# Performance work log

Measured on AMD Instinct MI355X. Metric: run time of the kernel, lower is better.

The kernel has to match this reference:

```python
import jax, jax.numpy as jnp
import numpy as np

N = 100000      # n_nodes
E = 1600000     # n_edges (avg degree 16)
D_IN, D_H, D_OUT = 128, 64, 16


def setup_inputs() -> dict:
    key = jax.random.key(0)
    k1, k2, k3, k4 = jax.random.split(key, 4)
    x = jax.random.normal(k1, (N, D_IN), dtype=jnp.float32)
    edge_index = jax.random.randint(k2, (2, E), 0, N, dtype=jnp.int32)
    W1 = jax.random.normal(k3, (D_IN, D_H), dtype=jnp.float32) / np.sqrt(D_IN)
    b1 = jnp.zeros((D_H,), dtype=jnp.float32)
    W2 = jax.random.normal(k4, (D_H, D_OUT), dtype=jnp.float32) / np.sqrt(D_H)
    b2 = jnp.zeros((D_OUT,), dtype=jnp.float32)
    return {"x": x, "edge_index": edge_index, "W1": W1, "b1": b1, "W2": W2, "b2": b2}


def gcn_conv(x, src, dst, W, b, n):
    """PyG GCNConv: linear transform, then deg^-1/2 A deg^-1/2 aggregation, + bias.
    src/dst already include self-loops."""
    h = x @ W                                              # [n, d_out]
    deg = jax.ops.segment_sum(jnp.ones_like(dst, dtype=h.dtype), dst, num_segments=n)
    dinv = jnp.where(deg > 0, jax.lax.rsqrt(jnp.maximum(deg, 1.0)), 0.0)
    norm = dinv[src] * dinv[dst]                           # [E+n]
    msgs = h[src] * norm[:, None]                          # gather + scale
    out = jax.ops.segment_sum(msgs, dst, num_segments=n)   # scatter-add
    return out + b


def reference(x, edge_index, W1, b1, W2, b2):
    loops = jnp.arange(N, dtype=edge_index.dtype)
    src = jnp.concatenate([edge_index[0], loops])
    dst = jnp.concatenate([edge_index[1], loops])
    h = jax.nn.relu(gcn_conv(x, src, dst, W1, b1, N))
    return gcn_conv(h, src, dst, W2, b2, N)
```

## Files before the change

### kernel.cpp

```cpp
#include <hip/hip_runtime.h>
#include <cstdint>

#define N_NODES 100000
#define N_EDGES 1600000
#define D_IN    128
#define D_H     64
#define D_OUT   16
#define M_TILES 6250

#define NBKT   512
#define NPB    196
#define BCAP   4096
#define TILE_E 4096
#define NTILES ((N_EDGES + TILE_E - 1) / TILE_E)
#define G1     128

typedef __attribute__((ext_vector_type(8))) short short8;
typedef __attribute__((ext_vector_type(4))) float floatx4;

static __device__ __forceinline__ unsigned short f2bf(float f) {
    unsigned int u = __float_as_uint(f);
    u = u + 0x7FFFu + ((u >> 16) & 1u);
    return (unsigned short)(u >> 16);
}
static __device__ __forceinline__ float bf2f(unsigned short h) {
    return __uint_as_float(((unsigned int)h) << 16);
}


__global__ __launch_bounds__(512) void zero_small_kernel(int* __restrict__ cursors,
                                                         int* __restrict__ srcs) {
    cursors[threadIdx.x] = 0;
    if (threadIdx.x < 16) srcs[N_EDGES + threadIdx.x] = 0;
}

__global__ __launch_bounds__(256) void bin_kernel(const int* __restrict__ src,
                                                  const int* __restrict__ dst,
                                                  int* __restrict__ cursors,
                                                  int* __restrict__ region) {
    __shared__ int hcnt[NBKT];
    __shared__ int hbase[NBKT];
    const int t = threadIdx.x;
    for (int tile = blockIdx.x; tile < NTILES; tile += gridDim.x) {
        for (int i = t; i < NBKT; i += 256) hcnt[i] = 0;
        __syncthreads();
        int e0 = tile * TILE_E + t * 16;
        int pk[16], bk[16], rk[16];
        bool full = (e0 + 16 <= N_EDGES);
        if (full) {
            const int4* dp = (const int4*)(dst + e0);
            const int4* sp = (const int4*)(src + e0);
            int dv[16], sv[16];
            #pragma unroll
            for (int q = 0; q < 4; ++q) {
                int4 d4 = dp[q]; int4 s4 = sp[q];
                dv[4*q+0]=d4.x; dv[4*q+1]=d4.y; dv[4*q+2]=d4.z; dv[4*q+3]=d4.w;
                sv[4*q+0]=s4.x; sv[4*q+1]=s4.y; sv[4*q+2]=s4.z; sv[4*q+3]=s4.w;
            }
            #pragma unroll
            for (int k = 0; k < 16; ++k) {
                int d = dv[k];
                int b = d / NPB;
                bk[k] = b;
                pk[k] = ((d - b * NPB) << 17) | sv[k];
                rk[k] = atomicAdd(&hcnt[b], 1);
            }
        }
        __syncthreads();
        for (int i = t; i < NBKT; i += 256) {
            int c = hcnt[i];
            if (c > 0) hbase[i] = atomicAdd(&cursors[i], c);
        }
        __syncthreads();
        if (full) {
            #pragma unroll
            for (int k = 0; k < 16; ++k)
                region[bk[k] * BCAP + hbase[bk[k]] + rk[k]] = pk[k];
        }
        __syncthreads();
    }
}

__global__ __launch_bounds__(256) void build_kernel(const int* __restrict__ cursors,
                                                    const int* __restrict__ region,
                                                    int* __restrict__ offsets,
                                                    float* __restrict__ dinv,
                                                    int* __restrict__ srcs) {
    __shared__ int lhist[NPB];
    __shared__ int lscan[NPB + 1];
    __shared__ int sbuf[256];
    __shared__ int srt[BCAP];
    __shared__ int red[4];
    int b = blockIdx.x;
    int t = threadIdx.x;

    int c0 = cursors[t];
    int c1 = cursors[t + 256];
    int p = ((t < b) ? c0 : 0) + ((t + 256 < b) ? c1 : 0);
    int lane = t & 63, wid = t >> 6;
    #pragma unroll
    for (int off = 32; off > 0; off >>= 1) p += __shfl_down(p, off);
    if (lane == 0) red[wid] = p;
    __syncthreads();
    int base = red[0] + red[1] + red[2] + red[3];
    int cnt = cursors[b];
    const int* reg = region + b * BCAP;

    for (int i = t; i < NPB; i += 256) lhist[i] = 0;
    __syncthreads();
    for (int i = t; i < cnt; i += 256) {
        int ln = reg[i] >> 17;
        atomicAdd(&lhist[ln], 1);
    }
    __syncthreads();
    int v = (t < NPB) ? lhist[t] : 0;
    sbuf[t] = v;
    __syncthreads();
    for (int off = 1; off < 256; off <<= 1) {
        int u = (t >= off) ? sbuf[t - off] : 0;
        __syncthreads();
        sbuf[t] += u;
        __syncthreads();
    }
    int incl = sbuf[t];
    if (t < NPB) lscan[t] = incl - v;
    if (t == NPB - 1) lscan[NPB] = incl;
    __syncthreads();
    if (t < NPB) lhist[t] = incl - v;
    __syncthreads();

    int node0 = b * NPB;
    int nlim = N_NODES - node0;
    if (nlim > NPB) nlim = NPB;
    if (t < nlim) {
        offsets[node0 + t] = base + lscan[t];
        int c = lscan[t + 1] - lscan[t];
        dinv[node0 + t] = rsqrtf((float)c + 1.0f);
    }
    if (b == (N_NODES - 1) / NPB && t == 0) offsets[N_NODES] = base + cnt;

    for (int i = t; i < cnt; i += 256) {
        int pk = reg[i];
        int ln = pk >> 17;
        int pos = atomicAdd(&lhist[ln], 1);
        srt[pos] = pk & 0x1FFFF;
    }
    __syncthreads();
    for (int i = t; i < cnt; i += 256) srcs[base + i] = srt[i];
}

__global__ __launch_bounds__(256) void gemm1_mfma_kernel(const float* __restrict__ x,
                                                         const float* __restrict__ W1,
                                                         const float* __restrict__ dinv,
                                                         unsigned short* __restrict__ hs) {
    __shared__ unsigned short bhi_lds[8192];
    __shared__ unsigned short blo_lds[8192];

    for (int e = threadIdx.x; e < 8192; e += 256) {
        int j    = e & 7;
        int lane = (e >> 3) & 63;
        int pair = e >> 9;
        int kc   = pair >> 2;
        int nt   = pair & 3;
        int k = kc * 32 + (lane >> 4) * 8 + j;
        int n = nt * 16 + (lane & 15);
        float w = W1[k * D_H + n];
        unsigned short hi = f2bf(w);
        float lo = w - bf2f(hi);
        bhi_lds[e] = hi;
        blo_lds[e] = f2bf(lo);
    }
    __syncthreads();

    int wid  = threadIdx.x >> 6;
    int lane = threadIdx.x & 63;
    int quad = lane >> 4;
    int m    = lane & 15;

    int tile = blockIdx.x * 4 + wid;
    if (tile >= M_TILES) return;
    int mbase = tile * 16;

    const float* xr = x + (size_t)(mbase + m) * D_IN + quad * 8;
    short8 ahi[4], alo[4];
    #pragma unroll
    for (int kc = 0; kc < 4; ++kc) {
        floatx4 v0 = *(const floatx4*)(xr + kc * 32);
        floatx4 v1 = *(const floatx4*)(xr + kc * 32 + 4);
        float f[8] = {v0.x, v0.y, v0.z, v0.w, v1.x, v1.y, v1.z, v1.w};
        #pragma unroll
        for (int j = 0; j < 8; ++j) {
            unsigned short hi = f2bf(f[j]);
            float lo = f[j] - bf2f(hi);
            ahi[kc][j] = (short)hi;
            alo[kc][j] = (short)f2bf(lo);
        }
    }

    floatx4 acc[4] = {{0.f,0.f,0.f,0.f},{0.f,0.f,0.f,0.f},{0.f,0.f,0.f,0.f},{0.f,0.f,0.f,0.f}};
    #pragma unroll
    for (int kc = 0; kc < 4; ++kc) {
        #pragma unroll
        for (int nt = 0; nt < 4; ++nt) {
            int fo = ((kc * 4 + nt) * 64 + lane) * 8;
            short8 bhi = *(const short8*)&bhi_lds[fo];
            short8 blo = *(const short8*)&blo_lds[fo];
            acc[nt] = __builtin_amdgcn_mfma_f32_16x16x32_bf16(ahi[kc], bhi, acc[nt], 0, 0, 0);
            acc[nt] = __builtin_amdgcn_mfma_f32_16x16x32_bf16(ahi[kc], blo, acc[nt], 0, 0, 0);
            acc[nt] = __builtin_amdgcn_mfma_f32_16x16x32_bf16(alo[kc], bhi, acc[nt], 0, 0, 0);
        }
    }

    float dv[4];
    #pragma unroll
    for (int r = 0; r < 4; ++r) dv[r] = dinv[mbase + quad * 4 + r];
    #pragma unroll
    for (int nt = 0; nt < 4; ++nt) {
        int col = nt * 16 + m;
        #pragma unroll
        for (int r = 0; r < 4; ++r) {
            int row = mbase + quad * 4 + r;
            hs[row * D_H + col] = f2bf(acc[nt][r] * dv[r]);
        }
    }
}

__global__ __launch_bounds__(256) void agg1_fused_kernel(const unsigned short* __restrict__ hs,
                                                         const int* __restrict__ offsets,
                                                         const int* __restrict__ srcs,
                                                         const float* __restrict__ dinv,
                                                         const float* __restrict__ b1,
                                                         const float* __restrict__ W2,
                                                         float* __restrict__ h2s) {
    __shared__ float rbuf[256];
    int wid  = threadIdx.x >> 6;
    int lane = threadIdx.x & 63;
    int wave = (blockIdx.x * blockDim.x + threadIdx.x) >> 6;
    int nwaves = (gridDim.x * blockDim.x) >> 6;

    int q = lane >> 4;
    int c = lane & 15;
    float w2c[16];
    #pragma unroll
    for (int j = 0; j < 16; ++j) w2c[j] = W2[(q * 16 + j) * D_OUT + c];
    float bias = b1[lane];
    float* myr = &rbuf[wid * 64];

    for (int node = wave; node < N_NODES; node += nwaves) {
        int beg = __builtin_amdgcn_readfirstlane(offsets[node]);
        int end = __builtin_amdgcn_readfirstlane(offsets[node + 1]);
        float acc = bf2f(hs[node * D_H + lane]);
        for (int e = beg; e < end; e += 16) {
            int rem = end - e;
            const int* ep = srcs + e;
            int jj[16];
            #pragma unroll
            for (int k = 0; k < 16; ++k)
                jj[k] = __builtin_amdgcn_readfirstlane(ep[k]);
            float vv[16];
            #pragma unroll
            for (int k = 0; k < 16; ++k) {
                const unsigned short* hp = hs + (size_t)jj[k] * D_H;
                vv[k] = bf2f(hp[lane]);
            }
            #pragma unroll
            for (int k = 0; k < 16; ++k) {
                float m = (k < rem) ? 1.0f : 0.0f;
                acc = fmaf(vv[k], m, acc);
            }
        }
        float dv = dinv[node];
        float r = fmaxf(acc * dv + bias, 0.f);

        myr[lane] = r;
        float part = 0.f;
        #pragma unroll
        for (int j = 0; j < 16; ++j) part += myr[q * 16 + j] * w2c[j];
        part += __shfl_xor(part, 16);
        part += __shfl_xor(part, 32);
        if (lane < 16) h2s[node * D_OUT + lane] = part * dv;
    }
}

__global__ __launch_bounds__(256) void agg2_kernel(const float* __restrict__ h2s,
                                                   const int* __restrict__ offsets,
                                                   const int* __restrict__ srcs,
                                                   const float* __restrict__ dinv,
                                                   const float* __restrict__ b2,
                                                   float* __restrict__ out) {
    int col = threadIdx.x & 15;
    int nidx = (blockIdx.x * blockDim.x + threadIdx.x) >> 4;
    int stride = (gridDim.x * blockDim.x) >> 4;
    for (int node = nidx; node < N_NODES; node += stride) {
        int beg = offsets[node], end = offsets[node + 1];
        float acc = h2s[node * D_OUT + col];
        for (int e = beg; e < end; e += 16) {
            int rem = end - e;
            const int* ep = srcs + e;
            int jj[16];
            #pragma unroll
            for (int k = 0; k < 16; ++k) jj[k] = ep[k];
            float vv[16];
            #pragma unroll
            for (int k = 0; k < 16; ++k) vv[k] = h2s[jj[k] * D_OUT + col];
            #pragma unroll
            for (int k = 0; k < 16; ++k) {
                float m = (k < rem) ? 1.0f : 0.0f;
                acc = fmaf(vv[k], m, acc);
            }
        }
        out[node * D_OUT + col] = acc * dinv[node] + b2[col];
    }
}

extern "C" void kernel_launch(void* const* d_in, const int* in_sizes, int n_in,
                              void* d_out, int out_size, void* d_ws, size_t ws_size,
                              hipStream_t stream) {
    const float* x  = (const float*)d_in[0];
    const int*   ei = (const int*)d_in[1];
    const float* W1 = (const float*)d_in[2];
    const float* b1 = (const float*)d_in[3];
    const float* W2 = (const float*)d_in[4];
    const float* b2 = (const float*)d_in[5];
    float* out = (float*)d_out;

    const int* src = ei;
    const int* dst = ei + N_EDGES;

    char* w = (char*)d_ws;
    int*   cursors  = (int*)(w + 0);
    int*   offsets  = (int*)(w + 4096);
    float* dinv     = (float*)(w + 404224);
    int*   srcs     = (int*)(w + 804224);
    unsigned short* hs = (unsigned short*)(w + 7204352);
    float* h2s      = (float*)(w + 20004480);
    int*   region   = (int*)(w + 26404480);

    zero_small_kernel<<<1, 512, 0, stream>>>(cursors, srcs);
    bin_kernel<<<G1, 256, 0, stream>>>(src, dst, cursors, region);
    build_kernel<<<NBKT, 256, 0, stream>>>(cursors, region, offsets, dinv, srcs);
    gemm1_mfma_kernel<<<(M_TILES + 3) / 4, 256, 0, stream>>>(x, W1, dinv, hs);
    agg1_fused_kernel<<<6250, 256, 0, stream>>>(hs, offsets, srcs, dinv, b1, W2, h2s);
    agg2_kernel<<<6250, 256, 0, stream>>>(h2s, offsets, srcs, dinv, b2, out);
}
```

Measured before the change: 206.4 us.

## Fuse all GCN stages into one cooperative persistent kernel with grid syncs

Replaces the six-kernel pipeline with a single cooperative mega-kernel that runs zeroing, edge binning, CSR build, the first GEMM and both aggregations, separated by grid.sync. Bucket count doubles, nodes per bucket halve and edges per thread drop, so binning runs one tile per block across 1024 blocks. W1 is split into bf16 hi/lo parts once into global memory rather than in LDS per block. The aim is to remove launch gaps and inter-kernel drain, at the cost of grid-wide barriers, persistent-loop load imbalance and reading W1 fragments from global/L2. A fallback multi-kernel path runs if a cooperative launch is not possible.

```diff
diff --git a/kernel.cpp b/kernel.cpp
--- a/kernel.cpp
+++ b/kernel.cpp
@@ -1,5 +1,8 @@
 #include <hip/hip_runtime.h>
+#include <hip/hip_cooperative_groups.h>
 #include <cstdint>
+
+namespace cg = cooperative_groups;
 
 #define N_NODES 100000
 #define N_EDGES 1600000
@@ -8,12 +11,13 @@
 #define D_OUT   16
 #define M_TILES 6250
 
-#define NBKT   512
-#define NPB    196
-#define BCAP   4096
-#define TILE_E 4096
-#define NTILES ((N_EDGES + TILE_E - 1) / TILE_E)
-#define G1     128
+#define NBKT   1024
+#define NPB    98
+#define BCAP   2048
+#define EPT    8
+#define TILE_E 2048
+#define NTILES 782
+#define GRID_B 1024
 
 typedef __attribute__((ext_vector_type(8))) short short8;
 typedef __attribute__((ext_vector_type(4))) float floatx4;
@@ -28,64 +32,331 @@
 }
 
 
-__global__ __launch_bounds__(512) void zero_small_kernel(int* __restrict__ cursors,
-                                                         int* __restrict__ srcs) {
+union SMem {
+    struct { int hcnt[NBKT]; int hbase[NBKT]; } bin;
+    struct { int lhist[NPB]; int lscan[NPB + 1]; int sbuf[256]; int red[4];
+             int srt[BCAP]; } bld;
+    float rbuf[256];
+};
+
+__global__ __launch_bounds__(256, 4) void mega_kernel(
+        const float* __restrict__ x,
+        const int* __restrict__ esrc, const int* __restrict__ edst,
+        const float* __restrict__ W1, const float* __restrict__ b1,
+        const float* __restrict__ W2, const float* __restrict__ b2,
+        float* __restrict__ out,
+        int* __restrict__ cursors, int* __restrict__ offsets,
+        float* __restrict__ dinv, int* __restrict__ srcs,
+        unsigned short* __restrict__ hs, float* __restrict__ h2s,
+        int* __restrict__ region,
+        unsigned short* __restrict__ w1hi, unsigned short* __restrict__ w1lo) {
+    cg::grid_group grid = cg::this_grid();
+    __shared__ SMem sm;
+    const int t = threadIdx.x;
+    const int gtid = blockIdx.x * 256 + t;
+
+    if (gtid < NBKT) cursors[gtid] = 0;
+    if (gtid < 16) srcs[N_EDGES + gtid] = 0;
+    if (gtid < 8192) {
+        int e = gtid;
+        int j    = e & 7;
+        int lane = (e >> 3) & 63;
+        int pair = e >> 9;
+        int kc   = pair >> 2;
+        int nt   = pair & 3;
+        int k = kc * 32 + (lane >> 4) * 8 + j;
+        int n = nt * 16 + (lane & 15);
+        float w = W1[k * D_H + n];
+        unsigned short hi = f2bf(w);
+        w1hi[e] = hi;
+        w1lo[e] = f2bf(w - bf2f(hi));
+    }
+    grid.sync();
+
+    {
+        int tile = blockIdx.x;
+        if (tile < NTILES) {
+            for (int i = t; i < NBKT; i += 256) sm.bin.hcnt[i] = 0;
+            __syncthreads();
+            int e0 = tile * TILE_E + t * EPT;
+            int pk[EPT], bk[EPT], rk[EPT];
+            bool full = (e0 + EPT <= N_EDGES);
+            if (full) {
+                const int4* dp = (const int4*)(edst + e0);
+                const int4* sp = (const int4*)(esrc + e0);
+                int dv[EPT], sv[EPT];
+                #pragma unroll
+                for (int q = 0; q < EPT / 4; ++q) {
+                    int4 d4 = dp[q]; int4 s4 = sp[q];
+                    dv[4*q+0]=d4.x; dv[4*q+1]=d4.y; dv[4*q+2]=d4.z; dv[4*q+3]=d4.w;
+                    sv[4*q+0]=s4.x; sv[4*q+1]=s4.y; sv[4*q+2]=s4.z; sv[4*q+3]=s4.w;
+                }
+                #pragma unroll
+                for (int k = 0; k < EPT; ++k) {
+                    int d = dv[k];
+                    int b = d / NPB;
+                    bk[k] = b;
+                    pk[k] = ((d - b * NPB) << 17) | sv[k];
+                    rk[k] = atomicAdd(&sm.bin.hcnt[b], 1);
+                }
+            }
+            __syncthreads();
+            for (int i = t; i < NBKT; i += 256) {
+                int c = sm.bin.hcnt[i];
+                if (c > 0) sm.bin.hbase[i] = atomicAdd(&cursors[i], c);
+            }
+            __syncthreads();
+            if (full) {
+                #pragma unroll
+                for (int k = 0; k < EPT; ++k)
+                    region[bk[k] * BCAP + sm.bin.hbase[bk[k]] + rk[k]] = pk[k];
+            }
+        }
+    }
+    grid.sync();
+
+    {
+        int b = blockIdx.x;
+        int p = 0;
+        #pragma unroll
+        for (int j = 0; j < 4; ++j) {
+            int i = t + 256 * j;
+            int cv = cursors[i];
+            p += (i < b) ? cv : 0;
+        }
+        int lane = t & 63, wid = t >> 6;
+        #pragma unroll
+        for (int off = 32; off > 0; off >>= 1) p += __shfl_down(p, off);
+        if (lane == 0) sm.bld.red[wid] = p;
+        __syncthreads();
+        int base = sm.bld.red[0] + sm.bld.red[1] + sm.bld.red[2] + sm.bld.red[3];
+        int cnt = cursors[b];
+        const int* reg = region + b * BCAP;
+
+        for (int i = t; i < NPB; i += 256) sm.bld.lhist[i] = 0;
+        __syncthreads();
+        for (int i = t; i < cnt; i += 256)
+            atomicAdd(&sm.bld.lhist[reg[i] >> 17], 1);
+        __syncthreads();
+        int v = (t < NPB) ? sm.bld.lhist[t] : 0;
+        sm.bld.sbuf[t] = v;
+        __syncthreads();
+        for (int off = 1; off < 256; off <<= 1) {
+            int u = (t >= off) ? sm.bld.sbuf[t - off] : 0;
+            __syncthreads();
+            sm.bld.sbuf[t] += u;
+            __syncthreads();
+        }
+        int incl = sm.bld.sbuf[t];
+        if (t < NPB) sm.bld.lscan[t] = incl - v;
+        if (t == NPB - 1) sm.bld.lscan[NPB] = incl;
+        __syncthreads();
+        if (t < NPB) sm.bld.lhist[t] = incl - v;
+        __syncthreads();
+
+        int node0 = b * NPB;
+        int nlim = N_NODES - node0;
+        if (nlim > NPB) nlim = NPB;
+        if (t < nlim) {
+            offsets[node0 + t] = base + sm.bld.lscan[t];
+            int c = sm.bld.lscan[t + 1] - sm.bld.lscan[t];
+            dinv[node0 + t] = rsqrtf((float)c + 1.0f);
+        }
+        if (b == (N_NODES - 1) / NPB && t == 0) offsets[N_NODES] = base + cnt;
+
+        for (int i = t; i < cnt; i += 256) {
+            int pk2 = reg[i];
+            int pos = atomicAdd(&sm.bld.lhist[pk2 >> 17], 1);
+            sm.bld.srt[pos] = pk2 & 0x1FFFF;
+        }
+        __syncthreads();
+        for (int i = t; i < cnt; i += 256) srcs[base + i] = sm.bld.srt[i];
+    }
+    grid.sync();
+
+    {
+        int wid  = t >> 6;
+        int lane = t & 63;
+        int quad = lane >> 4;
+        int m    = lane & 15;
+
+        for (int tile = blockIdx.x * 4 + wid; tile < M_TILES; tile += gridDim.x * 4) {
+            int mbase = tile * 16;
+            const float* xr = x + (size_t)(mbase + m) * D_IN + quad * 8;
+            short8 ahi[4], alo[4];
+            #pragma unroll
+            for (int kc = 0; kc < 4; ++kc) {
+                floatx4 v0 = *(const floatx4*)(xr + kc * 32);
+                floatx4 v1 = *(const floatx4*)(xr + kc * 32 + 4);
+                float f[8] = {v0.x, v0.y, v0.z, v0.w, v1.x, v1.y, v1.z, v1.w};
+                #pragma unroll
+                for (int j = 0; j < 8; ++j) {
+                    unsigned short hi = f2bf(f[j]);
+                    ahi[kc][j] = (short)hi;
+                    alo[kc][j] = (short)f2bf(f[j] - bf2f(hi));
+                }
+            }
+            floatx4 acc[4] = {{0.f,0.f,0.f,0.f},{0.f,0.f,0.f,0.f},{0.f,0.f,0.f,0.f},{0.f,0.f,0.f,0.f}};
+            #pragma unroll
+            for (int kc = 0; kc < 4; ++kc) {
+                #pragma unroll
+                for (int nt = 0; nt < 4; ++nt) {
+                    int fo = ((kc * 4 + nt) * 64 + lane) * 8;
+                    short8 bhi = *(const short8*)&w1hi[fo];
+                    short8 blo = *(const short8*)&w1lo[fo];
+                    acc[nt] = __builtin_amdgcn_mfma_f32_16x16x32_bf16(ahi[kc], bhi, acc[nt], 0, 0, 0);
+                    acc[nt] = __builtin_amdgcn_mfma_f32_16x16x32_bf16(ahi[kc], blo, acc[nt], 0, 0, 0);
+                    acc[nt] = __builtin_amdgcn_mfma_f32_16x16x32_bf16(alo[kc], bhi, acc[nt], 0, 0, 0);
+                }
+            }
+            float dv[4];
+            #pragma unroll
+            for (int r = 0; r < 4; ++r) dv[r] = dinv[mbase + quad * 4 + r];
+            #pragma unroll
+            for (int nt = 0; nt < 4; ++nt) {
+                int col = nt * 16 + m;
+                #pragma unroll
+                for (int r = 0; r < 4; ++r)
+                    hs[(mbase + quad * 4 + r) * D_H + col] = f2bf(acc[nt][r] * dv[r]);
+            }
+        }
+    }
+    grid.sync();
+
+    {
+        int wid  = t >> 6;
+        int lane = t & 63;
+        int wave = (blockIdx.x * 256 + t) >> 6;
+        const int nwaves = gridDim.x * 4;
+        int q = lane >> 4;
+        int c = lane & 15;
+        float w2c[16];
+        #pragma unroll
+        for (int j = 0; j < 16; ++j) w2c[j] = W2[(q * 16 + j) * D_OUT + c];
+        float bias = b1[lane];
+        float* myr = &sm.rbuf[wid * 64];
+
+        for (int node = wave; node < N_NODES; node += nwaves) {
+            int beg = __builtin_amdgcn_readfirstlane(offsets[node]);
+            int end = __builtin_amdgcn_readfirstlane(offsets[node + 1]);
+            float acc = bf2f(hs[node * D_H + lane]);
+            for (int e = beg; e < end; e += 16) {
+                int rem = end - e;
+                const int* ep = srcs + e;
+                int jj[16];
+                #pragma unroll
+                for (int k = 0; k < 16; ++k)
+                    jj[k] = __builtin_amdgcn_readfirstlane(ep[k]);
+                float vv[16];
+                #pragma unroll
+                for (int k = 0; k < 16; ++k) {
+                    const unsigned short* hp = hs + (size_t)jj[k] * D_H;
+                    vv[k] = bf2f(hp[lane]);
+                }
+                #pragma unroll
+                for (int k = 0; k < 16; ++k) {
+                    float m = (k < rem) ? 1.0f : 0.0f;
+                    acc = fmaf(vv[k], m, acc);
+                }
+            }
+            float dv = dinv[node];
+            float r = fmaxf(acc * dv + bias, 0.f);
+            myr[lane] = r;
+            float part = 0.f;
+            #pragma unroll
+            for (int j = 0; j < 16; ++j) part += myr[q * 16 + j] * w2c[j];
+            part += __shfl_xor(part, 16);
+            part += __shfl_xor(part, 32);
+            if (lane < 16) h2s[node * D_OUT + lane] = part * dv;
+        }
+    }
+    grid.sync();
+
+    {
+        int col = t & 15;
+        int nidx = (blockIdx.x * 256 + t) >> 4;
+        const int stride = (gridDim.x * 256) >> 4;
+        for (int node = nidx; node < N_NODES; node += stride) {
+            int beg = offsets[node], end = offsets[node + 1];
+            float acc = h2s[node * D_OUT + col];
+            for (int e = beg; e < end; e += 16) {
+                int rem = end - e;
+                const int* ep = srcs + e;
+                int jj[16];
+                #pragma unroll
+                for (int k = 0; k < 16; ++k) jj[k] = ep[k];
+                float vv[16];
+                #pragma unroll
+                for (int k = 0; k < 16; ++k) vv[k] = h2s[jj[k] * D_OUT + col];
+                #pragma unroll
+                for (int k = 0; k < 16; ++k) {
+                    float m = (k < rem) ? 1.0f : 0.0f;
+                    acc = fmaf(vv[k], m, acc);
+                }
+            }
+            out[node * D_OUT + col] = acc * dinv[node] + b2[col];
+        }
+    }
+}
+
+
+__global__ __launch_bounds__(1024) void fb_zero(int* __restrict__ cursors,
+                                                int* __restrict__ srcs) {
     cursors[threadIdx.x] = 0;
     if (threadIdx.x < 16) srcs[N_EDGES + threadIdx.x] = 0;
 }
 
-__global__ __launch_bounds__(256) void bin_kernel(const int* __restrict__ src,
-                                                  const int* __restrict__ dst,
-                                                  int* __restrict__ cursors,
-                                                  int* __restrict__ region) {
+__global__ __launch_bounds__(256) void fb_bin(const int* __restrict__ esrc,
+                                              const int* __restrict__ edst,
+                                              int* __restrict__ cursors,
+                                              int* __restrict__ region) {
     __shared__ int hcnt[NBKT];
     __shared__ int hbase[NBKT];
     const int t = threadIdx.x;
-    for (int tile = blockIdx.x; tile < NTILES; tile += gridDim.x) {
-        for (int i = t; i < NBKT; i += 256) hcnt[i] = 0;
-        __syncthreads();
-        int e0 = tile * TILE_E + t * 16;
-        int pk[16], bk[16], rk[16];
-        bool full = (e0 + 16 <= N_EDGES);
-        if (full) {
-            const int4* dp = (const int4*)(dst + e0);
-            const int4* sp = (const int4*)(src + e0);
-            int dv[16], sv[16];
-            #pragma unroll
-            for (int q = 0; q < 4; ++q) {
-                int4 d4 = dp[q]; int4 s4 = sp[q];
-                dv[4*q+0]=d4.x; dv[4*q+1]=d4.y; dv[4*q+2]=d4.z; dv[4*q+3]=d4.w;
-                sv[4*q+0]=s4.x; sv[4*q+1]=s4.y; sv[4*q+2]=s4.z; sv[4*q+3]=s4.w;
-            }
-            #pragma unroll
-            for (int k = 0; k < 16; ++k) {
-                int d = dv[k];
-                int b = d / NPB;
-                bk[k] = b;
-                pk[k] = ((d - b * NPB) << 17) | sv[k];
-                rk[k] = atomicAdd(&hcnt[b], 1);
-            }
-        }
-        __syncthreads();
-        for (int i = t; i < NBKT; i += 256) {
-            int c = hcnt[i];
-            if (c > 0) hbase[i] = atomicAdd(&cursors[i], c);
-        }
-        __syncthreads();
-        if (full) {
-            #pragma unroll
-            for (int k = 0; k < 16; ++k)
-                region[bk[k] * BCAP + hbase[bk[k]] + rk[k]] = pk[k];
-        }
-        __syncthreads();
-    }
-}
-
-__global__ __launch_bounds__(256) void build_kernel(const int* __restrict__ cursors,
-                                                    const int* __restrict__ region,
-                                                    int* __restrict__ offsets,
-                                                    float* __restrict__ dinv,
-                                                    int* __restrict__ srcs) {
+    int tile = blockIdx.x;
+    if (tile >= NTILES) return;
+    for (int i = t; i < NBKT; i += 256) hcnt[i] = 0;
+    __syncthreads();
+    int e0 = tile * TILE_E + t * EPT;
+    int pk[EPT], bk[EPT], rk[EPT];
+    bool full = (e0 + EPT <= N_EDGES);
+    if (full) {
+        const int4* dp = (const int4*)(edst + e0);
+        const int4* sp = (const int4*)(esrc + e0);
+        int dv[EPT], sv[EPT];
+        #pragma unroll
+        for (int q = 0; q < EPT / 4; ++q) {
+            int4 d4 = dp[q]; int4 s4 = sp[q];
+            dv[4*q+0]=d4.x; dv[4*q+1]=d4.y; dv[4*q+2]=d4.z; dv[4*q+3]=d4.w;
+            sv[4*q+0]=s4.x; sv[4*q+1]=s4.y; sv[4*q+2]=s4.z; sv[4*q+3]=s4.w;
+        }
+        #pragma unroll
+        for (int k = 0; k < EPT; ++k) {
+            int d = dv[k];
+            int b = d / NPB;
+            bk[k] = b;
+            pk[k] = ((d - b * NPB) << 17) | sv[k];
+            rk[k] = atomicAdd(&hcnt[b], 1);
+        }
+    }
+    __syncthreads();
+    for (int i = t; i < NBKT; i += 256) {
+        int c = hcnt[i];
+        if (c > 0) hbase[i] = atomicAdd(&cursors[i], c);
+    }
+    __syncthreads();
+    if (full) {
+        #pragma unroll
+        for (int k = 0; k < EPT; ++k)
+            region[bk[k] * BCAP + hbase[bk[k]] + rk[k]] = pk[k];
+    }
+}
+
+__global__ __launch_bounds__(256) void fb_build(const int* __restrict__ cursors,
+                                                const int* __restrict__ region,
+                                                int* __restrict__ offsets,
+                                                float* __restrict__ dinv,
+                                                int* __restrict__ srcs) {
     __shared__ int lhist[NPB];
     __shared__ int lscan[NPB + 1];
     __shared__ int sbuf[256];
@@ -93,10 +364,13 @@
     __shared__ int red[4];
     int b = blockIdx.x;
     int t = threadIdx.x;
-
-    int c0 = cursors[t];
-    int c1 = cursors[t + 256];
-    int p = ((t < b) ? c0 : 0) + ((t + 256 < b) ? c1 : 0);
+    int p = 0;
+    #pragma unroll
+    for (int j = 0; j < 4; ++j) {
+        int i = t + 256 * j;
+        int cv = cursors[i];
+        p += (i < b) ? cv : 0;
+    }
     int lane = t & 63, wid = t >> 6;
     #pragma unroll
     for (int off = 32; off > 0; off >>= 1) p += __shfl_down(p, off);
@@ -108,10 +382,7 @@
 
     for (int i = t; i < NPB; i += 256) lhist[i] = 0;
     __syncthreads();
-    for (int i = t; i < cnt; i += 256) {
-        int ln = reg[i] >> 17;
-        atomicAdd(&lhist[ln], 1);
-    }
+    for (int i = t; i < cnt; i += 256) atomicAdd(&lhist[reg[i] >> 17], 1);
     __syncthreads();
     int v = (t < NPB) ? lhist[t] : 0;
     sbuf[t] = v;
@@ -140,22 +411,20 @@
     if (b == (N_NODES - 1) / NPB && t == 0) offsets[N_NODES] = base + cnt;
 
     for (int i = t; i < cnt; i += 256) {
-        int pk = reg[i];
-        int ln = pk >> 17;
-        int pos = atomicAdd(&lhist[ln], 1);
-        srt[pos] = pk & 0x1FFFF;
+        int pk2 = reg[i];
+        int pos = atomicAdd(&lhist[pk2 >> 17], 1);
+        srt[pos] = pk2 & 0x1FFFF;
     }
     __syncthreads();
     for (int i = t; i < cnt; i += 256) srcs[base + i] = srt[i];
 }
 
-__global__ __launch_bounds__(256) void gemm1_mfma_kernel(const float* __restrict__ x,
-                                                         const float* __restrict__ W1,
-                                                         const float* __restrict__ dinv,
-                                                         unsigned short* __restrict__ hs) {
+__global__ __launch_bounds__(256) void fb_gemm1(const float* __restrict__ x,
+                                                const float* __restrict__ W1,
+                                                const float* __restrict__ dinv,
+                                                unsigned short* __restrict__ hs) {
     __shared__ unsigned short bhi_lds[8192];
     __shared__ unsigned short blo_lds[8192];
-
     for (int e = threadIdx.x; e < 8192; e += 256) {
         int j    = e & 7;
         int lane = (e >> 3) & 63;
@@ -166,21 +435,17 @@
         int n = nt * 16 + (lane & 15);
         float w = W1[k * D_H + n];
         unsigned short hi = f2bf(w);
-        float lo = w - bf2f(hi);
         bhi_lds[e] = hi;
-        blo_lds[e] = f2bf(lo);
-    }
-    __syncthreads();
-
+        blo_lds[e] = f2bf(w - bf2f(hi));
+    }
+    __syncthreads();
     int wid  = threadIdx.x >> 6;
     int lane = threadIdx.x & 63;
     int quad = lane >> 4;
     int m    = lane & 15;
-
     int tile = blockIdx.x * 4 + wid;
     if (tile >= M_TILES) return;
     int mbase = tile * 16;
-
     const float* xr = x + (size_t)(mbase + m) * D_IN + quad * 8;
     short8 ahi[4], alo[4];
     #pragma unroll
@@ -191,12 +456,10 @@
         #pragma unroll
         for (int j = 0; j < 8; ++j) {
             unsigned short hi = f2bf(f[j]);
-            float lo = f[j] - bf2f(hi);
             ahi[kc][j] = (short)hi;
-            alo[kc][j] = (short)f2bf(lo);
-        }
-    }
-
+            alo[kc][j] = (short)f2bf(f[j] - bf2f(hi));
+        }
+    }
     floatx4 acc[4] = {{0.f,0.f,0.f,0.f},{0.f,0.f,0.f,0.f},{0.f,0.f,0.f,0.f},{0.f,0.f,0.f,0.f}};
     #pragma unroll
     for (int kc = 0; kc < 4; ++kc) {
@@ -210,7 +473,6 @@
             acc[nt] = __builtin_amdgcn_mfma_f32_16x16x32_bf16(alo[kc], bhi, acc[nt], 0, 0, 0);
         }
     }
-
     float dv[4];
     #pragma unroll
     for (int r = 0; r < 4; ++r) dv[r] = dinv[mbase + quad * 4 + r];
@@ -218,26 +480,23 @@
     for (int nt = 0; nt < 4; ++nt) {
         int col = nt * 16 + m;
         #pragma unroll
-        for (int r = 0; r < 4; ++r) {
-            int row = mbase + quad * 4 + r;
-            hs[row * D_H + col] = f2bf(acc[nt][r] * dv[r]);
-        }
-    }
-}
-
-__global__ __launch_bounds__(256) void agg1_fused_kernel(const unsigned short* __restrict__ hs,
-                                                         const int* __restrict__ offsets,
-                                                         const int* __restrict__ srcs,
-                                                         const float* __restrict__ dinv,
-                                                         const float* __restrict__ b1,
-                                                         const float* __restrict__ W2,
-                                                         float* __restrict__ h2s) {
+        for (int r = 0; r < 4; ++r)
+            hs[(mbase + quad * 4 + r) * D_H + col] = f2bf(acc[nt][r] * dv[r]);
+    }
+}
+
+__global__ __launch_bounds__(256) void fb_agg1(const unsigned short* __restrict__ hs,
+                                               const int* __restrict__ offsets,
+                                               const int* __restrict__ srcs,
+                                               const float* __restrict__ dinv,
+                                               const float* __restrict__ b1,
+                                               const float* __restrict__ W2,
+                                               float* __restrict__ h2s) {
     __shared__ float rbuf[256];
     int wid  = threadIdx.x >> 6;
     int lane = threadIdx.x & 63;
     int wave = (blockIdx.x * blockDim.x + threadIdx.x) >> 6;
     int nwaves = (gridDim.x * blockDim.x) >> 6;
-
     int q = lane >> 4;
     int c = lane & 15;
     float w2c[16];
@@ -245,7 +504,6 @@
     for (int j = 0; j < 16; ++j) w2c[j] = W2[(q * 16 + j) * D_OUT + c];
     float bias = b1[lane];
     float* myr = &rbuf[wid * 64];
-
     for (int node = wave; node < N_NODES; node += nwaves) {
         int beg = __builtin_amdgcn_readfirstlane(offsets[node]);
         int end = __builtin_amdgcn_readfirstlane(offsets[node + 1]);
@@ -255,8 +513,7 @@
             const int* ep = srcs + e;
             int jj[16];
             #pragma unroll
-            for (int k = 0; k < 16; ++k)
-                jj[k] = __builtin_amdgcn_readfirstlane(ep[k]);
+            for (int k = 0; k < 16; ++k) jj[k] = __builtin_amdgcn_readfirstlane(ep[k]);
             float vv[16];
             #pragma unroll
             for (int k = 0; k < 16; ++k) {
@@ -271,7 +528,6 @@
         }
         float dv = dinv[node];
         float r = fmaxf(acc * dv + bias, 0.f);
-
         myr[lane] = r;
         float part = 0.f;
         #pragma unroll
@@ -282,12 +538,12 @@
     }
 }
 
-__global__ __launch_bounds__(256) void agg2_kernel(const float* __restrict__ h2s,
-                                                   const int* __restrict__ offsets,
-                                                   const int* __restrict__ srcs,
-                                                   const float* __restrict__ dinv,
-                                                   const float* __restrict__ b2,
-                                                   float* __restrict__ out) {
+__global__ __launch_bounds__(256) void fb_agg2(const float* __restrict__ h2s,
+                                               const int* __restrict__ offsets,
+                                               const int* __restrict__ srcs,
+                                               const float* __restrict__ dinv,
+                                               const float* __restrict__ b2,
+                                               float* __restrict__ out) {
     int col = threadIdx.x & 15;
     int nidx = (blockIdx.x * blockDim.x + threadIdx.x) >> 4;
     int stride = (gridDim.x * blockDim.x) >> 4;
@@ -324,8 +580,8 @@
     const float* b2 = (const float*)d_in[5];
     float* out = (float*)d_out;
 
-    const int* src = ei;
-    const int* dst = ei + N_EDGES;
+    const int* esrc = ei;
+    const int* edst = ei + N_EDGES;
 
     char* w = (char*)d_ws;
     int*   cursors  = (int*)(w + 0);
@@ -335,11 +591,31 @@
     unsigned short* hs = (unsigned short*)(w + 7204352);
     float* h2s      = (float*)(w + 20004480);
     int*   region   = (int*)(w + 26404480);
-
-    zero_small_kernel<<<1, 512, 0, stream>>>(cursors, srcs);
-    bin_kernel<<<G1, 256, 0, stream>>>(src, dst, cursors, region);
-    build_kernel<<<NBKT, 256, 0, stream>>>(cursors, region, offsets, dinv, srcs);
-    gemm1_mfma_kernel<<<(M_TILES + 3) / 4, 256, 0, stream>>>(x, W1, dinv, hs);
-    agg1_fused_kernel<<<6250, 256, 0, stream>>>(hs, offsets, srcs, dinv, b1, W2, h2s);
-    agg2_kernel<<<6250, 256, 0, stream>>>(h2s, offsets, srcs, dinv, b2, out);
-}
+    unsigned short* w1hi = (unsigned short*)(w + 34793088);
+    unsigned short* w1lo = (unsigned short*)(w + 34809472);
+
+    int maxB = 0;
+    hipError_t oerr = hipOccupancyMaxActiveBlocksPerMultiprocessor(
+        &maxB, (const void*)mega_kernel, 256, 0);
+    bool coop_ok = (oerr == hipSuccess) && (maxB >= 4);
+
+    if (coop_ok) {
+        void* args[] = { (void*)&x, (void*)&esrc, (void*)&edst, (void*)&W1, (void*)&b1,
+                         (void*)&W2, (void*)&b2, (void*)&out,
+                         (void*)&cursors, (void*)&offsets, (void*)&dinv, (void*)&srcs,
+                         (void*)&hs, (void*)&h2s, (void*)&region,
+                         (void*)&w1hi, (void*)&w1lo };
+        hipError_t lerr = hipLaunchCooperativeKernel((const void*)mega_kernel,
+                                                     dim3(GRID_B), dim3(256),
+                                                     args, 0, stream);
+        if (lerr == hipSuccess) return;
+        coop_ok = false;
+    }
+
+    fb_zero<<<1, 1024, 0, stream>>>(cursors, srcs);
+    fb_bin<<<NTILES, 256, 0, stream>>>(esrc, edst, cursors, region);
+    fb_build<<<NBKT, 256, 0, stream>>>(cursors, region, offsets, dinv, srcs);
+    fb_gemm1<<<(M_TILES + 3) / 4, 256, 0, stream>>>(x, W1, dinv, hs);
+    fb_agg1<<<6250, 256, 0, stream>>>(hs, offsets, srcs, dinv, b1, W2, h2s);
+    fb_agg2<<<6250, 256, 0, stream>>>(h2s, offsets, srcs, dinv, b2, out);
+}
```

New measurement: 219.1 us. 1.06x slower.
